# Performance work log

Hardware: AMD Instinct MI355X
Metric: run time of the kernel (lower is better)

Reference implementation:

```python
import jax, jax.numpy as jnp
import numpy as np

B, C, H, W = 8, 512, 64, 64
CQ = C // 8  # query/key channels; must equal H==W for the mask broadcast to be valid


def _len_mask(n, length, dtype):
    keep = jnp.arange(n) < length
    return (keep[:, None] & keep[None, :]).astype(dtype)  # [n, n]


def setup_inputs() -> dict:
    key = jax.random.key(0)
    ks = jax.random.split(key, 10)
    s = lambda fan: 1.0 / np.sqrt(fan)
    return {
        "x1": jax.random.normal(ks[0], (B, C, H, W), jnp.float32),
        "x2": jax.random.normal(ks[1], (B, C, H, W), jnp.float32),
        "x3": jax.random.normal(ks[2], (B, C, H, W), jnp.float32),
        "Wq": jax.random.normal(ks[3], (CQ, C), jnp.float32) * s(C),
        "bq": jax.random.normal(ks[4], (CQ,), jnp.float32) * s(C),
        "Wk": jax.random.normal(ks[5], (CQ, C), jnp.float32) * s(C),
        "bk": jax.random.normal(ks[6], (CQ,), jnp.float32) * s(C),
        "Wv": jax.random.normal(ks[7], (C, C), jnp.float32) * s(C),
        "bv": jax.random.normal(ks[8], (C,), jnp.float32) * s(C),
        "gamma": jnp.asarray(0.5, jnp.float32),  # torch init is 0; nonzero to exercise the path
        "length": 32,
    }


def reference(x1, x2, x3, Wq, bq, Wk, bk, Wv, bv, gamma, length):
    b, c, h, w = x1.shape
    dt = x1.dtype
    # 1x1 convs as channel GEMMs
    q = jnp.einsum("bchw,oc->bohw", x1, Wq) + bq[None, :, None, None]  # [B,CQ,H,W]
    k = jnp.einsum("bchw,oc->bohw", x2, Wk) + bk[None, :, None, None]
    v = jnp.einsum("bchw,oc->bohw", x3, Wv) + bv[None, :, None, None]  # [B,C,H,W]

    mH = _len_mask(h, length, dt)  # [H,H] (CQ==H)
    mW = _len_mask(w, length, dt)  # [W,W] (CQ==W)

    # Column (H) attention branch
    qH = jnp.transpose(q, (0, 3, 2, 1)) * mH  # [B,W,H,CQ]
    kH = jnp.transpose(k, (0, 3, 1, 2)) * mH  # [B,W,CQ,H]
    eH = jnp.einsum("bwhc,bwcg->bwhg", qH, kH)  # [B,W,H,H]
    eH = jnp.where(jnp.eye(h, dtype=bool), -jnp.inf, eH)  # diagonal -inf trick
    eH = jnp.transpose(eH, (0, 2, 1, 3))  # [B,H,W,H]

    # Row (W) attention branch
    qW = jnp.transpose(q, (0, 2, 3, 1)) * mW  # [B,H,W,CQ]
    kW = jnp.transpose(k, (0, 2, 1, 3)) * mW  # [B,H,CQ,W]
    eW = jnp.einsum("bhwc,bhcg->bhwg", qW, kW)  # [B,H,W,W]

    att = jax.nn.softmax(jnp.concatenate([eH, eW], axis=3), axis=3)  # [B,H,W,H+W]
    attH = jnp.transpose(att[..., :h], (0, 2, 1, 3))  # [B,W,H,H]
    attW = att[..., h:]  # [B,H,W,W]

    vH = jnp.transpose(v, (0, 3, 1, 2))  # [B,W,C,H]
    vW = jnp.transpose(v, (0, 2, 1, 3))  # [B,H,C,W]
    outH = jnp.einsum("bwcj,bwij->bwci", vH, attH)  # [B,W,C,H]
    outH = jnp.transpose(outH, (0, 2, 3, 1))  # [B,C,H,W]
    outW = jnp.einsum("bhcj,bhij->bhci", vW, attW)  # [B,H,C,W]
    outW = jnp.transpose(outW, (0, 2, 1, 3))  # [B,C,H,W]

    return gamma * (outH + outW) + x1
```

## Files before the change

### kernel.cpp

```cpp
#include <hip/hip_runtime.h>
#include <math.h>

#define CH 512
#define CQ 64
#define HH 64
#define WW 64
#define PP (HH*WW)
#define BB 8

typedef __bf16 bf16x8 __attribute__((ext_vector_type(8)));
typedef __bf16 bf16x4 __attribute__((ext_vector_type(4)));
typedef float  f32x4  __attribute__((ext_vector_type(4)));

__device__ __forceinline__ unsigned lds_off(const void* p) {
  return (unsigned)(size_t)(__attribute__((address_space(3))) const void*)p;
}
__device__ __forceinline__ bf16x4 ds_tr16(unsigned addr) {
  bf16x4 r;
  asm volatile("ds_read_b64_tr_b16 %0, %1" : "=v"(r) : "v"(addr));
  return r;
}

template<int FM, int FN, bool SPLIT, int NOUT, typename OutT>
__global__ __launch_bounds__(256) void proj_mfma_kernel(
    const float* __restrict__ X0, const float* __restrict__ W0,
    const float* __restrict__ bias0, OutT* __restrict__ Y0,
    const float* __restrict__ X1, const float* __restrict__ W1,
    const float* __restrict__ bias1, OutT* __restrict__ Y1)
{
  constexpr int BM = 32 * FM;
  constexpr int BN = 32 * FN;
  constexpr int NS = SPLIT ? 2 : 1;
  constexpr int GA = BM / 64;
  constexpr int GB = BN / 64;
  __shared__ __align__(16) __bf16 As[2][NS][BM][40];
  __shared__ __align__(16) __bf16 Bs[2][NS][BN][40];

  const int tid = threadIdx.x;
  const int sel = blockIdx.z;
  const float* X    = sel ? X1 : X0;
  const float* W    = sel ? W1 : W0;
  const float* bias = sel ? bias1 : bias0;
  OutT* Y           = sel ? Y1 : Y0;

  const int mblk = blockIdx.x * BM;
  const int nblk = blockIdx.y * BN;
  const int b     = mblk >> 12;
  const int pbase = mblk & 4095;
  const float* Xb = X + (size_t)b * CH * PP;

  const int l  = tid & 63;
  const int wv = tid >> 6;
  const int wr = wv >> 1, wc = wv & 1;
  const int lm = l & 15, lk = l >> 4;

  int ma[GA], ka[GA];
  #pragma unroll
  for (int gi = 0; gi < GA; ++gi) {
    int g = tid + gi * 256;
    ma[gi] = g % BM;
    ka[gi] = (g / BM) * 8;
  }
  int nb_[GB], kb_[GB];
  #pragma unroll
  for (int gi = 0; gi < GB; ++gi) {
    int g = tid + gi * 256;
    nb_[gi] = g >> 2;
    kb_[gi] = (g & 3) * 8;
  }

  float ra0[GA][8], ra1[GA][8];
  float rb[GB][8];

  auto loadA = [&](float (&ra)[GA][8], int c0) {
    #pragma unroll
    for (int gi = 0; gi < GA; ++gi)
      #pragma unroll
      for (int jj = 0; jj < 8; ++jj)
        ra[gi][jj] = Xb[(size_t)(c0 + ka[gi] + jj) * PP + pbase + ma[gi]];
  };
  auto loadB = [&](int c0) {
    #pragma unroll
    for (int gi = 0; gi < GB; ++gi) {
      const float* src = W + (size_t)(nblk + nb_[gi]) * CH + c0 + kb_[gi];
      float4 f0 = *(const float4*)src;
      float4 f1 = *(const float4*)(src + 4);
      rb[gi][0]=f0.x; rb[gi][1]=f0.y; rb[gi][2]=f0.z; rb[gi][3]=f0.w;
      rb[gi][4]=f1.x; rb[gi][5]=f1.y; rb[gi][6]=f1.z; rb[gi][7]=f1.w;
    }
  };

  f32x4 acc[FM][FN];
  #pragma unroll
  for (int j = 0; j < FN; ++j) {
    float bvj = bias[nblk + wc*FN*16 + j*16 + lm];
    #pragma unroll
    for (int i = 0; i < FM; ++i) {
      acc[i][j][0] = bvj; acc[i][j][1] = bvj;
      acc[i][j][2] = bvj; acc[i][j][3] = bvj;
    }
  }

  auto phase = [&](int t, auto par_c, float (&ra)[GA][8]) {
    constexpr int PAR = decltype(par_c)::value;
    #pragma unroll
    for (int gi = 0; gi < GA; ++gi) {
      bf16x8 hv, lv;
      #pragma unroll
      for (int jj = 0; jj < 8; ++jj) {
        __bf16 hh = (__bf16)ra[gi][jj];
        hv[jj] = hh;
        if (SPLIT) lv[jj] = (__bf16)(ra[gi][jj] - (float)hh);
      }
      *(bf16x8*)&As[PAR][0][ma[gi]][ka[gi]] = hv;
      if (SPLIT) *(bf16x8*)&As[PAR][1][ma[gi]][ka[gi]] = lv;
    }
    #pragma unroll
    for (int gi = 0; gi < GB; ++gi) {
      bf16x8 hv, lv;
      #pragma unroll
      for (int jj = 0; jj < 8; ++jj) {
        __bf16 hh = (__bf16)rb[gi][jj];
        hv[jj] = hh;
        if (SPLIT) lv[jj] = (__bf16)(rb[gi][jj] - (float)hh);
      }
      *(bf16x8*)&Bs[PAR][0][nb_[gi]][kb_[gi]] = hv;
      if (SPLIT) *(bf16x8*)&Bs[PAR][1][nb_[gi]][kb_[gi]] = lv;
    }
    __syncthreads();
    if (t < 15) loadB((t+1)*32);
    if (t < 14) loadA(ra, (t+2)*32);
    bf16x8 af[NS][FM], bfr[NS][FN];
    #pragma unroll
    for (int s = 0; s < NS; ++s) {
      #pragma unroll
      for (int i = 0; i < FM; ++i)
        af[s][i] = *(const bf16x8*)&As[PAR][s][wr*FM*16 + i*16 + lm][lk*8];
      #pragma unroll
      for (int j = 0; j < FN; ++j)
        bfr[s][j] = *(const bf16x8*)&Bs[PAR][s][wc*FN*16 + j*16 + lm][lk*8];
    }
    #pragma unroll
    for (int i = 0; i < FM; ++i) {
      #pragma unroll
      for (int j = 0; j < FN; ++j) {
        acc[i][j] = __builtin_amdgcn_mfma_f32_16x16x32_bf16(
            af[0][i], bfr[0][j], acc[i][j], 0, 0, 0);
        if (SPLIT) {
          acc[i][j] = __builtin_amdgcn_mfma_f32_16x16x32_bf16(
              af[0][i], bfr[1][j], acc[i][j], 0, 0, 0);
          acc[i][j] = __builtin_amdgcn_mfma_f32_16x16x32_bf16(
              af[1][i], bfr[0][j], acc[i][j], 0, 0, 0);
        }
      }
    }
  };

  loadA(ra0, 0); loadB(0); loadA(ra1, 32);
  for (int tt = 0; tt < 8; ++tt) {
    phase(2*tt,     std::integral_constant<int,0>{}, ra0);
    phase(2*tt + 1, std::integral_constant<int,1>{}, ra1);
  }

  #pragma unroll
  for (int i = 0; i < FM; ++i) {
    #pragma unroll
    for (int j = 0; j < FN; ++j) {
      #pragma unroll
      for (int r = 0; r < 4; ++r) {
        int mg = mblk + wr*FM*16 + i*16 + lk*4 + r;
        int ng = nblk + wc*FN*16 + j*16 + lm;
        Y[(size_t)mg * NOUT + ng] = (OutT)acc[i][j][r];
      }
    }
  }
}

__global__ __launch_bounds__(256) void energyH_kernel(
    const float* __restrict__ qt, const float* __restrict__ kt,
    float* __restrict__ eH, const int* __restrict__ len_p)
{
  const int tid = threadIdx.x;
  const int w = blockIdx.x, b = blockIdx.y;
  int L = *len_p; L = L < 0 ? 0 : (L > 64 ? 64 : L);
  __shared__ float Qs[64][68];
  __shared__ float Ks[64][68];
  {
    const int c = tid & 63, hg = tid >> 6;
    const float* qb = qt + ((size_t)b * PP + w) * CQ + c;
    const float* kb = kt + ((size_t)b * PP + w) * CQ + c;
    #pragma unroll
    for (int r = 0; r < 16; ++r) {
      int h = hg*16 + r;
      Qs[h][c] = qb[(size_t)h * WW * CQ];
      Ks[h][c] = kb[(size_t)h * WW * CQ];
    }
  }
  __syncthreads();
  const int g  = tid & 63;
  const int wg = tid >> 6;
  float kreg[64];
  #pragma unroll
  for (int c = 0; c < 64; ++c) kreg[c] = (c < L) ? Ks[g][c] : 0.0f;
  const bool gok = (g < L);
  float* ab = eH + (((size_t)b * HH) * WW + w) * 64 + g;
  for (int r = 0; r < 16; ++r) {
    int h = wg*16 + r;
    float e = 0.0f;
    #pragma unroll
    for (int c4 = 0; c4 < 16; ++c4) {
      float4 q4 = *(const float4*)&Qs[h][4*c4];
      e += q4.x*kreg[4*c4+0] + q4.y*kreg[4*c4+1]
         + q4.z*kreg[4*c4+2] + q4.w*kreg[4*c4+3];
    }
    e = (gok && h < L) ? e : 0.0f;
    if (g == h) e = -INFINITY;
    ab[(size_t)h * WW * 64] = e;
  }
}

__global__ __launch_bounds__(256) void energyW_softmax_kernel(
    const float* __restrict__ qt, const float* __restrict__ kt,
    const float* __restrict__ eH,
    __bf16* __restrict__ attHb, __bf16* __restrict__ attWb,
    const int* __restrict__ len_p)
{
  const int tid = threadIdx.x;
  const int h = blockIdx.x, b = blockIdx.y;
  int L = *len_p; L = L < 0 ? 0 : (L > 64 ? 64 : L);
  __shared__ float Qs[64][68];
  __shared__ float Ks[64][68];
  {
    const int c = tid & 63, wg2 = tid >> 6;
    const float* qb = qt + ((size_t)b * PP + (size_t)h * WW) * CQ + c;
    const float* kb = kt + ((size_t)b * PP + (size_t)h * WW) * CQ + c;
    #pragma unroll
    for (int r = 0; r < 16; ++r) {
      int w = wg2*16 + r;
      Qs[w][c] = qb[(size_t)w * CQ];
      Ks[w][c] = kb[(size_t)w * CQ];
    }
  }
  __syncthreads();
  const int g  = tid & 63;
  const int wg = tid >> 6;
  float kreg[64];
  #pragma unroll
  for (int c = 0; c < 64; ++c) kreg[c] = (c < L) ? Ks[g][c] : 0.0f;
  const bool gok = (g < L);
  const float* ehb = eH + (((size_t)b * HH + h) * WW) * 64 + g;
  __bf16* ahb = attHb + (((size_t)b * HH + h) * WW) * 64 + g;
  __bf16* awb = attWb + (((size_t)b * HH + h) * WW) * 64 + g;
  for (int r = 0; r < 16; ++r) {
    int w = wg*16 + r;
    float e = 0.0f;
    #pragma unroll
    for (int c4 = 0; c4 < 16; ++c4) {
      float4 q4 = *(const float4*)&Qs[w][4*c4];
      e += q4.x*kreg[4*c4+0] + q4.y*kreg[4*c4+1]
         + q4.z*kreg[4*c4+2] + q4.w*kreg[4*c4+3];
    }
    e = (gok && w < L) ? e : 0.0f;
    float eh = ehb[(size_t)w * 64];
    float m = fmaxf(e, eh);
    #pragma unroll
    for (int d = 32; d > 0; d >>= 1) m = fmaxf(m, __shfl_xor(m, d, 64));
    float pe = __expf(e  - m);
    float ph = __expf(eh - m);
    float s = pe + ph;
    #pragma unroll
    for (int d = 32; d > 0; d >>= 1) s += __shfl_xor(s, d, 64);
    float inv = 1.0f / s;
    ahb[(size_t)w * 64] = (__bf16)(ph * inv);
    awb[(size_t)w * 64] = (__bf16)(pe * inv);
  }
}

__device__ __forceinline__ int vsub64_off(int j, int c) {
  int s  = j >> 5;
  int p  = (j >> 2) & 1;
  int t  = ((j & 31) >> 3) * 4 + (j & 3);
  return ((s*2 + p)*4 + (c >> 4))*256 + t*16 + (c & 15);
}

__global__ __launch_bounds__(256) void outH_mfma_kernel(
    const __bf16* __restrict__ attHb, const __bf16* __restrict__ vt,
    __bf16* __restrict__ oH)
{
  const int tid = threadIdx.x;
  const int w = blockIdx.x, cq = blockIdx.y, b = blockIdx.z;
  const int l = tid & 63, wv = tid >> 6;
  const int lm = l & 15, lk = l >> 4;

  __shared__ __align__(16) __bf16 Bs[4096];

  #pragma unroll
  for (int i = 0; i < 2; ++i) {
    int j  = i*32 + (tid >> 3);
    int c0 = (tid & 7) * 8;
    bf16x8 v8 = *(const bf16x8*)(vt + ((size_t)b*PP + (size_t)j*WW + w)*CH + cq*64 + c0);
    *(bf16x8*)&Bs[vsub64_off(j, c0)] = v8;
  }

  const int hrow = wv*16 + lm;
  const __bf16* ab = attHb + (((size_t)b*HH + hrow)*WW + w)*64;
  bf16x8 af[2];
  af[0] = *(const bf16x8*)(ab + lk*8);
  af[1] = *(const bf16x8*)(ab + 32 + lk*8);
  __syncthreads();

  const unsigned bs_base = lds_off(&Bs[0]);
  f32x4 acc[4];
  #pragma unroll
  for (int f = 0; f < 4; ++f) acc[f] = (f32x4){0.f,0.f,0.f,0.f};
  #pragma unroll
  for (int s = 0; s < 2; ++s) {
    bf16x8 bfr[4];
    #pragma unroll
    for (int f = 0; f < 4; ++f) {
      unsigned base = bs_base + (unsigned)((((s*2)*4 + f)*512)) + (unsigned)(l*8);
      bf16x4 t0 = ds_tr16(base);
      bf16x4 t1 = ds_tr16(base + 2048);
      bfr[f] = __builtin_shufflevector(t0, t1, 0,1,2,3,4,5,6,7);
    }
    asm volatile("s_waitcnt lgkmcnt(0)");
    __builtin_amdgcn_sched_barrier(0);
    #pragma unroll
    for (int f = 0; f < 4; ++f)
      acc[f] = __builtin_amdgcn_mfma_f32_16x16x32_bf16(af[s], bfr[f], acc[f], 0,0,0);
  }
  __bf16* ob = oH + (((size_t)b * HH) * WW + w) * CH + cq*64;
  #pragma unroll
  for (int f = 0; f < 4; ++f) {
    #pragma unroll
    for (int r = 0; r < 4; ++r) {
      int h = wv*16 + lk*4 + r;
      ob[(size_t)h * WW * CH + f*16 + lm] = (__bf16)acc[f][r];
    }
  }
}

__global__ __launch_bounds__(256) void outW_final_kernel(
    const __bf16* __restrict__ attWb, const __bf16* __restrict__ vt,
    const __bf16* __restrict__ oH,
    const float* __restrict__ x1, const float* __restrict__ gamma_p,
    float* __restrict__ out)
{
  const int tid = threadIdx.x;
  const int h = blockIdx.x, cq = blockIdx.y, b = blockIdx.z;
  const int l = tid & 63, wv = tid >> 6;
  const int lm = l & 15, lk = l >> 4;
  const float gamma = *gamma_p;

  __shared__ __align__(16) char smem[64*69*4];
  __bf16* Bs = (__bf16*)smem;
  typedef float ScRow[69];
  ScRow* Sc = (ScRow*)smem;

  #pragma unroll
  for (int i = 0; i < 2; ++i) {
    int j  = i*32 + (tid >> 3);
    int c0 = (tid & 7) * 8;
    bf16x8 v8 = *(const bf16x8*)(vt + ((size_t)b*PP + (size_t)h*WW + j)*CH + cq*64 + c0);
    *(bf16x8*)&Bs[vsub64_off(j, c0)] = v8;
  }

  const int wrow = wv*16 + lm;
  const __bf16* ab = attWb + (((size_t)b*HH + h)*WW + wrow)*64;
  bf16x8 af[2];
  af[0] = *(const bf16x8*)(ab + lk*8);
  af[1] = *(const bf16x8*)(ab + 32 + lk*8);

  const int wl = tid & 63, cg = tid >> 6;
  const __bf16* ohb = oH + ((((size_t)b*HH + h) * WW) + wl) * CH + cq*64 + cg*16;
  bf16x8 ohr[2];
  ohr[0] = *(const bf16x8*)(ohb);
  ohr[1] = *(const bf16x8*)(ohb + 8);
  float x1r[16];
  {
    const float* x1b = x1 + ((size_t)b*CH + cq*64 + cg*16)*PP + (size_t)h*WW + wl;
    #pragma unroll
    for (int r2 = 0; r2 < 16; ++r2)
      x1r[r2] = x1b[(size_t)r2 * PP];
  }
  __syncthreads();

  const unsigned bs_base = lds_off(&Bs[0]);
  f32x4 acc[4];
  #pragma unroll
  for (int f = 0; f < 4; ++f) acc[f] = (f32x4){0.f,0.f,0.f,0.f};
  #pragma unroll
  for (int s = 0; s < 2; ++s) {
    bf16x8 bfr[4];
    #pragma unroll
    for (int f = 0; f < 4; ++f) {
      unsigned base = bs_base + (unsigned)((((s*2)*4 + f)*512)) + (unsigned)(l*8);
      bf16x4 t0 = ds_tr16(base);
      bf16x4 t1 = ds_tr16(base + 2048);
      bfr[f] = __builtin_shufflevector(t0, t1, 0,1,2,3,4,5,6,7);
    }
    asm volatile("s_waitcnt lgkmcnt(0)");
    __builtin_amdgcn_sched_barrier(0);
    #pragma unroll
    for (int f = 0; f < 4; ++f)
      acc[f] = __builtin_amdgcn_mfma_f32_16x16x32_bf16(af[s], bfr[f], acc[f], 0,0,0);
  }

  __syncthreads();
  #pragma unroll
  for (int f = 0; f < 4; ++f) {
    #pragma unroll
    for (int r = 0; r < 4; ++r)
      Sc[wv*16 + lk*4 + r][f*16 + lm] = acc[f][r];
  }
  __syncthreads();
  {
    float* obp = out + ((size_t)b*CH + cq*64 + cg*16)*PP + (size_t)h*WW + wl;
    #pragma unroll
    for (int r2 = 0; r2 < 16; ++r2) {
      float oh = (float)ohr[r2 >> 3][r2 & 7];
      obp[(size_t)r2 * PP] = gamma * (Sc[wl][cg*16 + r2] + oh) + x1r[r2];
    }
  }
}

extern "C" void kernel_launch(void* const* d_in, const int* in_sizes, int n_in,
                              void* d_out, int out_size, void* d_ws, size_t ws_size,
                              hipStream_t stream)
{
  const float* x1 = (const float*)d_in[0];
  const float* x2 = (const float*)d_in[1];
  const float* x3 = (const float*)d_in[2];
  const float* Wq = (const float*)d_in[3];
  const float* bq = (const float*)d_in[4];
  const float* Wk = (const float*)d_in[5];
  const float* bk = (const float*)d_in[6];
  const float* Wv = (const float*)d_in[7];
  const float* bv = (const float*)d_in[8];
  const float* gamma = (const float*)d_in[9];
  const int*   len   = (const int*)d_in[10];
  float* out = (float*)d_out;

  float*  q_t   = (float*)d_ws;
  float*  k_t   = q_t + (size_t)BB * PP * CQ;
  float*  eH    = k_t + (size_t)BB * PP * CQ;
  __bf16* attHb = (__bf16*)(eH + (size_t)BB * PP * 64);
  __bf16* attWb = attHb + (size_t)BB * PP * 64;
  __bf16* v_t   = attWb + (size_t)BB * PP * 64;
  __bf16* oH    = v_t + (size_t)BB * PP * CH;

  dim3 blk(256);
  proj_mfma_kernel<4,4,false, CH, __bf16>
      <<<dim3(BB*PP/128, CH/128, 1), blk, 0, stream>>>(
          x3, Wv, bv, v_t,  x3, Wv, bv, v_t);
  proj_mfma_kernel<2,2,true, CQ, float>
      <<<dim3(BB*PP/64, 1, 2), blk, 0, stream>>>(
          x1, Wq, bq, q_t,  x2, Wk, bk, k_t);

  energyH_kernel<<<dim3(WW, BB), blk, 0, stream>>>(q_t, k_t, eH, len);
  energyW_softmax_kernel<<<dim3(HH, BB), blk, 0, stream>>>(q_t, k_t, eH, attHb, attWb, len);
  outH_mfma_kernel<<<dim3(WW, 8, BB), blk, 0, stream>>>(attHb, v_t, oH);
  outW_final_kernel<<<dim3(HH, 8, BB), blk, 0, stream>>>(attWb, v_t, oH, x1, gamma, out);
}
```

Baseline: 163.8 us.

## Merge Q/K/V projections into one launch and drop split-bf16 for Q/K

Replaces the two projection launches with a single kernel whose blocks select a role: one of four V column tiles, the Q projection, or the K projection, all sharing one LDS pool. The Q/K projection no longer uses the hi/lo bf16 split with three MFMAs per tile, and now uses plain bf16 with 128x64 tiles. This removes a kernel launch, lets the V and Q/K work run concurrently, and cuts MFMA and conversion work for Q/K. In exchange, Q and K lose precision before the softmax, which may affect accuracy.

Measured after the change: 158.5 us. 3.3% less time.

```diff
diff --git a/kernel.cpp b/kernel.cpp
--- a/kernel.cpp
+++ b/kernel.cpp
@@ -1,5 +1,6 @@
 #include <hip/hip_runtime.h>
 #include <math.h>
+#include <type_traits>
 
 #define CH 512
 #define CQ 64
@@ -21,30 +22,23 @@
   return r;
 }
 
-template<int FM, int FN, bool SPLIT, int NOUT, typename OutT>
-__global__ __launch_bounds__(256) void proj_mfma_kernel(
-    const float* __restrict__ X0, const float* __restrict__ W0,
-    const float* __restrict__ bias0, OutT* __restrict__ Y0,
-    const float* __restrict__ X1, const float* __restrict__ W1,
-    const float* __restrict__ bias1, OutT* __restrict__ Y1)
+template<int FM, int FN, int NOUT, typename OutT>
+__device__ __forceinline__ void proj_body(
+    __bf16* AsBase, __bf16* BsBase,
+    const float* __restrict__ X, const float* __restrict__ W,
+    const float* __restrict__ bias, OutT* __restrict__ Y,
+    int mblk, int nblk)
 {
   constexpr int BM = 32 * FM;
   constexpr int BN = 32 * FN;
-  constexpr int NS = SPLIT ? 2 : 1;
   constexpr int GA = BM / 64;
   constexpr int GB = BN / 64;
-  __shared__ __align__(16) __bf16 As[2][NS][BM][40];
-  __shared__ __align__(16) __bf16 Bs[2][NS][BN][40];
+  typedef __bf16 (*TileA)[BM][40];
+  typedef __bf16 (*TileB)[BN][40];
+  TileA As = (TileA)AsBase;
+  TileB Bs = (TileB)BsBase;
 
   const int tid = threadIdx.x;
-  const int sel = blockIdx.z;
-  const float* X    = sel ? X1 : X0;
-  const float* W    = sel ? W1 : W0;
-  const float* bias = sel ? bias1 : bias0;
-  OutT* Y           = sel ? Y1 : Y0;
-
-  const int mblk = blockIdx.x * BM;
-  const int nblk = blockIdx.y * BN;
   const int b     = mblk >> 12;
   const int pbase = mblk & 4095;
   const float* Xb = X + (size_t)b * CH * PP;
@@ -105,55 +99,34 @@
     constexpr int PAR = decltype(par_c)::value;
     #pragma unroll
     for (int gi = 0; gi < GA; ++gi) {
-      bf16x8 hv, lv;
+      bf16x8 hv;
       #pragma unroll
-      for (int jj = 0; jj < 8; ++jj) {
-        __bf16 hh = (__bf16)ra[gi][jj];
-        hv[jj] = hh;
-        if (SPLIT) lv[jj] = (__bf16)(ra[gi][jj] - (float)hh);
-      }
-      *(bf16x8*)&As[PAR][0][ma[gi]][ka[gi]] = hv;
-      if (SPLIT) *(bf16x8*)&As[PAR][1][ma[gi]][ka[gi]] = lv;
+      for (int jj = 0; jj < 8; ++jj) hv[jj] = (__bf16)ra[gi][jj];
+      *(bf16x8*)&As[PAR][ma[gi]][ka[gi]] = hv;
     }
     #pragma unroll
     for (int gi = 0; gi < GB; ++gi) {
-      bf16x8 hv, lv;
+      bf16x8 hv;
       #pragma unroll
-      for (int jj = 0; jj < 8; ++jj) {
-        __bf16 hh = (__bf16)rb[gi][jj];
-        hv[jj] = hh;
-        if (SPLIT) lv[jj] = (__bf16)(rb[gi][jj] - (float)hh);
-      }
-      *(bf16x8*)&Bs[PAR][0][nb_[gi]][kb_[gi]] = hv;
-      if (SPLIT) *(bf16x8*)&Bs[PAR][1][nb_[gi]][kb_[gi]] = lv;
+      for (int jj = 0; jj < 8; ++jj) hv[jj] = (__bf16)rb[gi][jj];
+      *(bf16x8*)&Bs[PAR][nb_[gi]][kb_[gi]] = hv;
     }
     __syncthreads();
     if (t < 15) loadB((t+1)*32);
     if (t < 14) loadA(ra, (t+2)*32);
-    bf16x8 af[NS][FM], bfr[NS][FN];
-    #pragma unroll
-    for (int s = 0; s < NS; ++s) {
-      #pragma unroll
-      for (int i = 0; i < FM; ++i)
-        af[s][i] = *(const bf16x8*)&As[PAR][s][wr*FM*16 + i*16 + lm][lk*8];
+    bf16x8 af[FM], bfr[FN];
+    #pragma unroll
+    for (int i = 0; i < FM; ++i)
+      af[i] = *(const bf16x8*)&As[PAR][wr*FM*16 + i*16 + lm][lk*8];
+    #pragma unroll
+    for (int j = 0; j < FN; ++j)
+      bfr[j] = *(const bf16x8*)&Bs[PAR][wc*FN*16 + j*16 + lm][lk*8];
+    #pragma unroll
+    for (int i = 0; i < FM; ++i)
       #pragma unroll
       for (int j = 0; j < FN; ++j)
-        bfr[s][j] = *(const bf16x8*)&Bs[PAR][s][wc*FN*16 + j*16 + lm][lk*8];
-    }
-    #pragma unroll
-    for (int i = 0; i < FM; ++i) {
-      #pragma unroll
-      for (int j = 0; j < FN; ++j) {
         acc[i][j] = __builtin_amdgcn_mfma_f32_16x16x32_bf16(
-            af[0][i], bfr[0][j], acc[i][j], 0, 0, 0);
-        if (SPLIT) {
-          acc[i][j] = __builtin_amdgcn_mfma_f32_16x16x32_bf16(
-              af[0][i], bfr[1][j], acc[i][j], 0, 0, 0);
-          acc[i][j] = __builtin_amdgcn_mfma_f32_16x16x32_bf16(
-              af[1][i], bfr[0][j], acc[i][j], 0, 0, 0);
-        }
-      }
-    }
+            af[i], bfr[j], acc[i][j], 0, 0, 0);
   };
 
   loadA(ra0, 0); loadB(0); loadA(ra1, 32);
@@ -173,6 +146,27 @@
         Y[(size_t)mg * NOUT + ng] = (OutT)acc[i][j][r];
       }
     }
+  }
+}
+
+__global__ __launch_bounds__(256) void proj_all_kernel(
+    const float* __restrict__ x3, const float* __restrict__ Wv,
+    const float* __restrict__ bv, __bf16* __restrict__ v_t,
+    const float* __restrict__ x1, const float* __restrict__ Wq,
+    const float* __restrict__ bq, float* __restrict__ q_t,
+    const float* __restrict__ x2, const float* __restrict__ Wk,
+    const float* __restrict__ bk, float* __restrict__ k_t)
+{
+  __shared__ __align__(16) __bf16 AsPool[2*128*40];
+  __shared__ __align__(16) __bf16 BsPool[2*128*40];
+  const int role = blockIdx.x;
+  const int mblk = blockIdx.y * 128;
+  if (role < 4) {
+    proj_body<4,4, CH, __bf16>(AsPool, BsPool, x3, Wv, bv, v_t, mblk, role*128);
+  } else if (role == 4) {
+    proj_body<4,2, CQ, float >(AsPool, BsPool, x1, Wq, bq, q_t, mblk, 0);
+  } else {
+    proj_body<4,2, CQ, float >(AsPool, BsPool, x2, Wk, bk, k_t, mblk, 0);
   }
 }
 
@@ -450,12 +444,8 @@
   __bf16* oH    = v_t + (size_t)BB * PP * CH;
 
   dim3 blk(256);
-  proj_mfma_kernel<4,4,false, CH, __bf16>
-      <<<dim3(BB*PP/128, CH/128, 1), blk, 0, stream>>>(
-          x3, Wv, bv, v_t,  x3, Wv, bv, v_t);
-  proj_mfma_kernel<2,2,true, CQ, float>
-      <<<dim3(BB*PP/64, 1, 2), blk, 0, stream>>>(
-          x1, Wq, bq, q_t,  x2, Wk, bk, k_t);
+  proj_all_kernel<<<dim3(6, BB*PP/128), blk, 0, stream>>>(
+      x3, Wv, bv, v_t,  x1, Wq, bq, q_t,  x2, Wk, bk, k_t);
 
   energyH_kernel<<<dim3(WW, BB), blk, 0, stream>>>(q_t, k_t, eH, len);
   energyW_softmax_kernel<<<dim3(HH, BB), blk, 0, stream>>>(q_t, k_t, eH, attHb, attWb, len);
```
